# Performance work log

Measured on AMD Instinct MI355X. Metric: run time of the kernel, lower is better.

The kernel has to match this reference:

```python
import jax, jax.numpy as jnp
import numpy as np

N = 50000; E = 800000
IN = 128; H = 4; D = 32; OH = H * D; AIN = 2 * IN
SCALE = float(1.0 / np.sqrt(IN))

def _ln(x, g, b):
    m = jnp.mean(x, -1, keepdims=True)
    v = jnp.mean((x - m) ** 2, -1, keepdims=True)
    return (x - m) * jax.lax.rsqrt(v + 1e-5) * g + b

def setup_inputs():
    keys = iter(jax.random.split(jax.random.key(0), 24))
    nrm = lambda shape, s=1.0: jax.random.normal(next(keys), shape, dtype=jnp.float32) * s
    inp = {}
    inp['x0'] = nrm((N, IN)); inp['x1'] = nrm((N, IN)); inp['x99'] = nrm((N, AIN))
    inp['feat0'] = jax.random.uniform(next(keys), (E, 2), dtype=jnp.float32)
    inp['feat1'] = jax.random.uniform(next(keys), (E, 2), dtype=jnp.float32)
    for nm, shape in [('Wq', (IN, OH)), ('Wk', (IN, OH)), ('Wv', (IN, OH)), ('Wo', (OH, OH)), ('Wffn', (IN, OH)), ('Waq', (AIN, OH)), ('Wak', (AIN, OH)), ('Wav', (AIN, OH)), ('Wao', (OH, OH)), ('Waffn', (AIN, OH))]:
        inp[nm] = nrm(shape, 0.05)
    for nm in ['bq', 'bk', 'bv', 'bo', 'bffn', 'baq', 'bak', 'bav', 'bao', 'baffn', 'ln_b', 'aln_b']:
        inp[nm] = jnp.zeros((OH,), jnp.float32)
    inp['ln_g'] = jnp.ones((OH,), jnp.float32); inp['aln_g'] = jnp.ones((OH,), jnp.float32)
    for nm in ['src0', 'dst0', 'src1', 'dst1']:
        inp[nm] = jax.random.randint(next(keys), (E,), 0, N, dtype=jnp.int32)
    return inp

def _forward(x0, x1, x99, feat0, feat1, Wq, bq, Wk, bk, Wv, bv, Wo, bo, Wffn, bffn, ln_g, ln_b, Waq, baq, Wak, bak, Wav, bav, Wao, bao, Waffn, baffn, aln_g, aln_b, src0, dst0, src1, dst1):
    proj = lambda x, W, b: (x @ W + b).reshape(x.shape[0], H, D)
    xs = (x0, x1)
    edges = ((src0, dst0, feat0), (src1, dst1, feat1))
    q = [proj(x, Wq, bq) for x in xs]   # per-v_id linears are shared
    k = [proj(x, Wk, bk) for x in xs]
    v = [proj(x, Wv, bv) for x in xs]
    q99 = proj(x99, Waq, baq); k99 = proj(x99, Wak, bak); v99 = proj(x99, Wav, bav)
    aggr_outs = []
    for i, (src, dst, feat) in enumerate(edges):  # loop over the 2 edge types (structural)
        f = feat[:, None, 0:1]  # [E,1,1] 'connect' edge weight
        s = jnp.sum(k[i][src] * q[i][dst], -1, keepdims=True) * f   # [E,H,1]
        s99 = jnp.sum(k99[src] * q99[dst], -1, keepdims=True) * f
        s = jnp.exp(jnp.clip(s * SCALE, -5.0, 5.0))
        s99 = jnp.exp(jnp.clip(s99 * SCALE, -5.0, 5.0))
        wv = jax.ops.segment_sum(v[i][src] * s, dst, num_segments=N)    # [N,H,D]
        z = jax.ops.segment_sum(s, dst, num_segments=N)                 # [N,H,1]
        wv99 = jax.ops.segment_sum(v99[src] * s99, dst, num_segments=N)
        z99 = jax.ops.segment_sum(s99, dst, num_segments=N)
        # per-v_id branch (h_dict in original; computed but not returned by the module)
        o = (wv / (z + 1.0)).reshape(N, OH) @ Wo + bo
        h = xs[i] @ Wffn + bffn + o
        h = h + _ln(h, ln_g, ln_b)
        # aggregated (node 99) branch -> returned as aggr_h_dict[v_id]
        ao = (wv99 / (z99 + 1.0)).reshape(N, OH) @ Wao + bao
        ah = x99 @ Waffn + baffn + ao
        ah = ah + _ln(ah, aln_g, aln_b)
        aggr_outs.append(ah)
    return tuple(aggr_outs)

def reference(x0, x1, x99, feat0, feat1, Wq, bq, Wk, bk, Wv, bv, Wo, bo, Wffn, bffn, ln_g, ln_b, Waq, baq, Wak, bak, Wav, bav, Wao, bao, Waffn, baffn, aln_g, aln_b, src0, dst0, src1, dst1):
    return _forward(x0, x1, x99, feat0, feat1, Wq, bq, Wk, bk, Wv, bv, Wo, bo, Wffn, bffn, ln_g, ln_b, Waq, baq, Wak, bak, Wav, bav, Wao, bao, Waffn, baffn, aln_g, aln_b, src0, dst0, src1, dst1)
```

## Files before the change

### kernel.cpp

```cpp
#include <hip/hip_runtime.h>
#include <math.h>

#define NN 50000
#define EE 800000
#define AIN 256
#define OH 128

#define NTOT  (2 * NN)
#define NB    391
#define CAP   5120

typedef __attribute__((ext_vector_type(8))) short bf16x8;
typedef __attribute__((ext_vector_type(4))) float f32x4;

static __device__ __forceinline__ unsigned short f2bf(float f) {
    union { float f; unsigned int u; } v; v.f = f;
    return (unsigned short)((v.u + 0x7FFFu + ((v.u >> 16) & 1u)) >> 16);
}
static __device__ __forceinline__ float bflo(unsigned int u) { return __uint_as_float(u << 16); }
static __device__ __forceinline__ float bfhi(unsigned int u) { return __uint_as_float(u & 0xFFFF0000u); }

static __device__ __forceinline__ float foldpair(float a, float b, int mask, int lane) {
    const bool hi = (lane & mask) != 0;
    const float keep = hi ? b : a;
    const float send = hi ? a : b;
    return keep + __shfl_xor(send, mask);
}

__global__ __launch_bounds__(256) void cvt_x_k(const float* __restrict__ x, unsigned short* __restrict__ xb)
{
    const int i = blockIdx.x * 256 + threadIdx.x;
    if (i >= NN * AIN / 4) return;
    const float4 v = ((const float4*)x)[i];
    ushort4 o;
    o.x = f2bf(v.x); o.y = f2bf(v.y); o.z = f2bf(v.z); o.w = f2bf(v.w);
    ((ushort4*)xb)[i] = o;
}

__global__ __launch_bounds__(256) void cvt_w_k(
    const float* __restrict__ Wq, const float* __restrict__ Wk,
    const float* __restrict__ Wv, const float* __restrict__ Wf,
    const float* __restrict__ Wo, unsigned short* __restrict__ Wt,
    unsigned short* __restrict__ Waot)
{
    const int n = blockIdx.x;
    const int k = threadIdx.x;
    if (n < 512) {
        const float* W = (n < 128) ? Wq : (n < 256) ? Wk : (n < 384) ? Wv : Wf;
        Wt[(size_t)n * 256 + k] = f2bf(W[(size_t)k * OH + (n & 127)]);
    } else {
        if (k < 128) Waot[(size_t)(n - 512) * 128 + k] = f2bf(Wo[(size_t)k * OH + (n - 512)]);
    }
}

__global__ __launch_bounds__(256) void qkvf_mfma_k(
    const unsigned short* __restrict__ xb,
    const unsigned short* __restrict__ Wt,
    const float* __restrict__ bq, const float* __restrict__ bk,
    const float* __restrict__ bv, const float* __restrict__ bf,
    float* __restrict__ qf, unsigned short* __restrict__ kv,
    unsigned short* __restrict__ ffnb, int M)
{
    __shared__ unsigned short As[128][40];
    __shared__ unsigned short Bs[128][40];
    const int tid  = threadIdx.x;
    const int lane = tid & 63;
    const int wave = tid >> 6;
    const int wr = wave >> 1, wc = wave & 1;
    const int quad = lane >> 4, m16 = lane & 15;
    const int row0 = blockIdx.x * 128;
    const int col0 = blockIdx.y * 128;

    f32x4 acc[4][4];
    #pragma unroll
    for (int i = 0; i < 4; ++i)
        #pragma unroll
        for (int j = 0; j < 4; ++j) acc[i][j] = 0.f;

    const int lr  = tid >> 1;
    const int lkh = (tid & 1) * 16;

    for (int kt = 0; kt < 256; kt += 32) {
        uint4 a0 = {0,0,0,0}, a1 = {0,0,0,0};
        const int grow = row0 + lr;
        if (grow < M) {
            const uint4* p = (const uint4*)(xb + (size_t)grow * 256 + kt + lkh);
            a0 = p[0]; a1 = p[1];
        }
        *(uint4*)&As[lr][lkh]     = a0;
        *(uint4*)&As[lr][lkh + 8] = a1;
        const uint4* wp = (const uint4*)(Wt + (size_t)(col0 + lr) * 256 + kt + lkh);
        *(uint4*)&Bs[lr][lkh]     = wp[0];
        *(uint4*)&Bs[lr][lkh + 8] = wp[1];
        __syncthreads();
        bf16x8 af[4], bfr[4];
        #pragma unroll
        for (int t = 0; t < 4; ++t) af[t]  = *(const bf16x8*)&As[wr * 64 + t * 16 + m16][quad * 8];
        #pragma unroll
        for (int t = 0; t < 4; ++t) bfr[t] = *(const bf16x8*)&Bs[wc * 64 + t * 16 + m16][quad * 8];
        #pragma unroll
        for (int i = 0; i < 4; ++i)
            #pragma unroll
            for (int j = 0; j < 4; ++j)
                acc[i][j] = __builtin_amdgcn_mfma_f32_16x16x32_bf16(af[i], bfr[j], acc[i][j], 0, 0, 0);
        __syncthreads();
    }

    const int y = blockIdx.y;
    const float* bias = (y == 0) ? bq : (y == 1) ? bk : (y == 2) ? bv : bf;

    if (y == 0) {
        #pragma unroll
        for (int i = 0; i < 4; ++i)
            #pragma unroll
            for (int j = 0; j < 4; ++j) {
                const int col = wc * 64 + j * 16 + m16;
                const float b = bias[col];
                #pragma unroll
                for (int r = 0; r < 4; ++r) {
                    const int row = row0 + wr * 64 + i * 16 + quad * 4 + r;
                    if (row < M) qf[(size_t)row * 128 + col] = acc[i][j][r] + b;
                }
            }
    } else {
        unsigned short* obase = (y == 3) ? ffnb : kv;
        const int ostride = (y == 3) ? 128 : 256;
        const int ocol    = (y == 2) ? 128 : 0;
        #pragma unroll
        for (int i = 0; i < 4; ++i)
            #pragma unroll
            for (int j = 0; j < 4; ++j) {
                const int col = wc * 64 + j * 16 + m16;
                const float b = bias[col];
                #pragma unroll
                for (int r = 0; r < 4; ++r) {
                    const int row = row0 + wr * 64 + i * 16 + quad * 4 + r;
                    if (row < M) obase[(size_t)row * ostride + ocol + col] = f2bf(acc[i][j][r] + b);
                }
            }
    }
}

__global__ __launch_bounds__(256) void binpass_k(
    const int* __restrict__ dst0, const int* __restrict__ dst1,
    const int* __restrict__ src0, const int* __restrict__ src1,
    const float* __restrict__ feat0, const float* __restrict__ feat1,
    int* __restrict__ cursor, uint2* __restrict__ stage)
{
    __shared__ int hcnt[NB], blkbase[NB], lcur[NB];
    const int tid = threadIdx.x;
    const long base = (long)blockIdx.x * 8192;

    for (int i = tid; i < NB; i += 256) { hcnt[i] = 0; lcur[i] = 0; }
    __syncthreads();

    for (int i = tid; i < 8192; i += 256) {
        const long e = base + i;
        if (e < 2L * EE) {
            const int nid = (e < EE) ? dst0[e] : NN + dst1[e - EE];
            atomicAdd(&hcnt[nid >> 8], 1);
        }
    }
    __syncthreads();
    for (int i = tid; i < NB; i += 256)
        if (hcnt[i]) blkbase[i] = atomicAdd(&cursor[i], hcnt[i]);
    __syncthreads();

    for (int i = tid; i < 8192; i += 256) {
        const long e = base + i;
        if (e < 2L * EE) {
            const bool a = (e < EE);
            const int ee = a ? (int)e : (int)(e - EE);
            const int nid = a ? dst0[ee] : NN + dst1[ee];
            const int s = a ? src0[ee] : src1[ee];
            const float f = a ? feat0[(size_t)ee * 2] : feat1[(size_t)ee * 2];
            const int bk = nid >> 8;
            const int r = atomicAdd(&lcur[bk], 1);
            uint2 rec;
            rec.x = __float_as_uint(f);
            rec.y = ((unsigned int)s << 8) | (unsigned int)(nid & 255);
            stage[(size_t)bk * CAP + blkbase[bk] + r] = rec;
        }
    }
}

__global__ __launch_bounds__(512) void bscan_k(const int* __restrict__ cursor, int* __restrict__ bbase)
{
    __shared__ int part[512];
    const int t = threadIdx.x;
    const int v = (t < NB) ? cursor[t] : 0;
    part[t] = v;
    __syncthreads();
    for (int st = 1; st < 512; st <<= 1) {
        int u = (t >= st) ? part[t - st] : 0;
        __syncthreads();
        part[t] += u;
        __syncthreads();
    }
    if (t < NB) bbase[t] = part[t] - v;
}

__global__ __launch_bounds__(256) void sortpass_k(
    const uint2* __restrict__ stage, const int* __restrict__ cursor,
    const int* __restrict__ bbase, uint2* __restrict__ erec,
    int* __restrict__ off, int* __restrict__ deg)
{
    __shared__ int h[256], eb[256], cur[256];
    const int b = blockIdx.x;
    const int t = threadIdx.x;
    const int cntb = cursor[b];
    const int obase = bbase[b];
    const uint2* sb = stage + (size_t)b * CAP;

    h[t] = 0; cur[t] = 0;
    __syncthreads();
    for (int i = t; i < cntb; i += 256) atomicAdd(&h[(int)(sb[i].y & 255u)], 1);
    __syncthreads();
    eb[t] = h[t];
    __syncthreads();
    for (int st = 1; st < 256; st <<= 1) {
        int u = (t >= st) ? eb[t - st] : 0;
        __syncthreads();
        eb[t] += u;
        __syncthreads();
    }
    const int incl = eb[t];
    __syncthreads();
    eb[t] = incl - h[t];
    __syncthreads();

    const int nid = b * 256 + t;
    if (nid < NTOT) {
        off[nid] = obase + eb[t];
        deg[nid] = h[t];
    }

    for (int i = t; i < cntb; i += 256) {
        const uint2 r = sb[i];
        const int loc = (int)(r.y & 255u);
        const int rk = atomicAdd(&cur[loc], 1);
        uint2 o;
        o.x = r.y >> 8;
        o.y = r.x;
        erec[obase + eb[loc] + rk] = o;
    }
}

__global__ __launch_bounds__(256) void aggregate_k(
    const float* __restrict__ qf, const unsigned short* __restrict__ kv,
    const uint2* __restrict__ erec,
    const int* __restrict__ off, const int* __restrict__ deg,
    unsigned short* __restrict__ att)
{
    const int nid = blockIdx.x * 4 + (threadIdx.x >> 6);
    if (nid >= NTOT) return;
    const int n = (nid >= NN) ? nid - NN : nid;
    const int lane = threadIdx.x & 63;
    const int start = off[nid];
    const int count = deg[nid];

    const float2 q2 = *(const float2*)&qf[(size_t)n * 128 + 2 * lane];
    const float qx = q2.x, qy = q2.y;

    float accx = 0.f, accy = 0.f, zp = 0.f;
    const float SCALE = 0.088388347648318447f;
    const int slot = lane & 7;

    for (int base = 0; base < count; base += 64) {
        const int m = min(64, count - base);
        const uint2 rr = erec[start + base + min(lane, m - 1)];
        for (int j0 = 0; j0 < m; j0 += 8) {
            const int mb = min(8, m - j0);
            unsigned int ku[8], vu[8];
            #pragma unroll
            for (int s = 0; s < 8; ++s) {
                const int src = __shfl((int)rr.x, j0 + s);
                const unsigned short* kp = kv + (size_t)src * 256 + 2 * lane;
                ku[s] = *(const unsigned int*)kp;
                vu[s] = *(const unsigned int*)(kp + 128);
            }
            float p[8];
            #pragma unroll
            for (int s = 0; s < 8; ++s)
                p[s] = fmaf(bfhi(ku[s]), qy, bflo(ku[s]) * qx);
            float r01 = foldpair(p[0], p[1], 1, lane);
            float r23 = foldpair(p[2], p[3], 1, lane);
            float r45 = foldpair(p[4], p[5], 1, lane);
            float r67 = foldpair(p[6], p[7], 1, lane);
            float r03 = foldpair(r01, r23, 2, lane);
            float r47 = foldpair(r45, r67, 2, lane);
            float r07 = foldpair(r03, r47, 4, lane);
            r07 += __shfl_xor(r07, 8);
            const float f = __int_as_float(__shfl((int)rr.y, j0 + slot));
            float sc = __expf(fminf(5.f, fmaxf(-5.f, r07 * f * SCALE)));
            if (slot >= mb) sc = 0.f;
            zp += sc;
            #pragma unroll
            for (int s = 0; s < 8; ++s) {
                const float scb = __shfl(sc, (lane & 48) + s);
                accx = fmaf(bflo(vu[s]), scb, accx);
                accy = fmaf(bfhi(vu[s]), scb, accy);
            }
        }
    }
    float z = zp;
    z += __shfl_xor(z, 1);
    z += __shfl_xor(z, 2);
    z += __shfl_xor(z, 4);

    const float inv = 1.f / (z + 1.f);
    const unsigned int o = ((unsigned int)f2bf(accy * inv) << 16) | (unsigned int)f2bf(accx * inv);
    *(unsigned int*)(att + (size_t)nid * 128 + 2 * lane) = o;
}

__global__ __launch_bounds__(256) void attn_out_mfma_k(
    const unsigned short* __restrict__ attAll, const unsigned short* __restrict__ Wt,
    const float* __restrict__ bo, const unsigned short* __restrict__ ffnb,
    const float* __restrict__ g, const float* __restrict__ bln,
    float* __restrict__ Yall, int M)
{
    __shared__ unsigned short As[128][40];
    __shared__ unsigned short Bs[128][40];
    __shared__ float rsum[2][128], rsq[2][128];
    __shared__ float meanar[128], invar[128];

    const unsigned short* att = attAll + (size_t)blockIdx.y * NN * 128;
    float* Y = Yall + (size_t)blockIdx.y * NN * 128;

    const int tid  = threadIdx.x;
    const int lane = tid & 63;
    const int wave = tid >> 6;
    const int wr = wave >> 1, wc = wave & 1;
    const int quad = lane >> 4, m16 = lane & 15;
    const int row0 = blockIdx.x * 128;

    f32x4 acc[4][4];
    #pragma unroll
    for (int i = 0; i < 4; ++i)
        #pragma unroll
        for (int j = 0; j < 4; ++j) acc[i][j] = 0.f;

    const int lr  = tid >> 1;
    const int lkh = (tid & 1) * 16;

    for (int kt = 0; kt < 128; kt += 32) {
        uint4 a0 = {0,0,0,0}, a1 = {0,0,0,0};
        const int grow = row0 + lr;
        if (grow < M) {
            const uint4* p = (const uint4*)(att + (size_t)grow * 128 + kt + lkh);
            a0 = p[0]; a1 = p[1];
        }
        *(uint4*)&As[lr][lkh]     = a0;
        *(uint4*)&As[lr][lkh + 8] = a1;
        const uint4* wp = (const uint4*)(Wt + (size_t)lr * 128 + kt + lkh);
        *(uint4*)&Bs[lr][lkh]     = wp[0];
        *(uint4*)&Bs[lr][lkh + 8] = wp[1];
        __syncthreads();
        bf16x8 af[4], bfr[4];
        #pragma unroll
        for (int t = 0; t < 4; ++t) af[t]  = *(const bf16x8*)&As[wr * 64 + t * 16 + m16][quad * 8];
        #pragma unroll
        for (int t = 0; t < 4; ++t) bfr[t] = *(const bf16x8*)&Bs[wc * 64 + t * 16 + m16][quad * 8];
        #pragma unroll
        for (int i = 0; i < 4; ++i)
            #pragma unroll
            for (int j = 0; j < 4; ++j)
                acc[i][j] = __builtin_amdgcn_mfma_f32_16x16x32_bf16(af[i], bfr[j], acc[i][j], 0, 0, 0);
        __syncthreads();
    }

    #pragma unroll
    for (int i = 0; i < 4; ++i) {
        #pragma unroll
        for (int r = 0; r < 4; ++r) {
            const int rl = wr * 64 + i * 16 + quad * 4 + r;
            const int grow = row0 + rl;
            float s = 0.f, q = 0.f;
            #pragma unroll
            for (int j = 0; j < 4; ++j) {
                const int col = wc * 64 + j * 16 + m16;
                float v = acc[i][j][r] + bo[col];
                if (grow < M) v += bflo(ffnb[(size_t)grow * 128 + col]);
                acc[i][j][r] = v;
                s += v; q += v * v;
            }
            #pragma unroll
            for (int mm = 1; mm <= 8; mm <<= 1) {
                s += __shfl_xor(s, mm, 16);
                q += __shfl_xor(q, mm, 16);
            }
            if (m16 == 0) { rsum[wc][rl] = s; rsq[wc][rl] = q; }
        }
    }
    __syncthreads();
    if (tid < 128) {
        const float s = rsum[0][tid] + rsum[1][tid];
        const float q = rsq[0][tid] + rsq[1][tid];
        const float mean = s * (1.f / 128.f);
        const float var  = q * (1.f / 128.f) - mean * mean;
        meanar[tid] = mean;
        invar[tid]  = rsqrtf(fmaxf(var, 0.f) + 1e-5f);
    }
    __syncthreads();

    #pragma unroll
    for (int i = 0; i < 4; ++i) {
        #pragma unroll
        for (int j = 0; j < 4; ++j) {
            const int col = wc * 64 + j * 16 + m16;
            const float gv = g[col], lv = bln[col];
            #pragma unroll
            for (int r = 0; r < 4; ++r) {
                const int rl = wr * 64 + i * 16 + quad * 4 + r;
                const int grow = row0 + rl;
                if (grow < M) {
                    const float v = acc[i][j][r];
                    Y[(size_t)grow * 128 + col] = v + (v - meanar[rl]) * invar[rl] * gv + lv;
                }
            }
        }
    }
}

extern "C" void kernel_launch(void* const* d_in, const int* in_sizes, int n_in,
                              void* d_out, int out_size, void* d_ws, size_t ws_size,
                              hipStream_t stream) {
    const float* x99   = (const float*)d_in[2];
    const float* feat0 = (const float*)d_in[3];
    const float* feat1 = (const float*)d_in[4];
    const float* Waq   = (const float*)d_in[10];
    const float* Wak   = (const float*)d_in[11];
    const float* Wav   = (const float*)d_in[12];
    const float* Wao   = (const float*)d_in[13];
    const float* Waffn = (const float*)d_in[14];
    const float* baq   = (const float*)d_in[20];
    const float* bak   = (const float*)d_in[21];
    const float* bav   = (const float*)d_in[22];
    const float* bao   = (const float*)d_in[23];
    const float* baffn = (const float*)d_in[24];
    const float* aln_b = (const float*)d_in[26];
    const float* aln_g = (const float*)d_in[28];
    const int* src0 = (const int*)d_in[29];
    const int* dst0 = (const int*)d_in[30];
    const int* src1 = (const int*)d_in[31];
    const int* dst1 = (const int*)d_in[32];

    unsigned short* xb   = (unsigned short*)d_ws;
    float*          qf   = (float*)(xb + (size_t)NN * 256);
    unsigned short* kv   = (unsigned short*)(qf + (size_t)NN * 128);
    unsigned short* ffnb = kv   + (size_t)NN * 256;
    unsigned short* att  = ffnb + (size_t)NN * 128;
    unsigned short* Wt   = att  + (size_t)NTOT * 128;
    unsigned short* Waot = Wt   + (size_t)512 * 256;
    int* cursor = (int*)(Waot + 128 * 128);
    int* bbase  = cursor + NB;
    int* off    = bbase + NB;
    int* deg    = off + NTOT;

    float* out = (float*)d_out;
    uint2* stage = (uint2*)d_out;
    uint2* erec  = stage + (size_t)NB * CAP;

    cvt_x_k<<<(NN * AIN / 4 + 255) / 256, 256, 0, stream>>>(x99, xb);
    cvt_w_k<<<640, 256, 0, stream>>>(Waq, Wak, Wav, Waffn, Wao, Wt, Waot);

    const int mtiles = (NN + 127) / 128;
    qkvf_mfma_k<<<dim3(mtiles, 4), 256, 0, stream>>>(xb, Wt, baq, bak, bav, baffn, qf, kv, ffnb, NN);

    hipMemsetAsync(cursor, 0, NB * sizeof(int), stream);
    binpass_k<<<(2 * EE + 8191) / 8192, 256, 0, stream>>>(
        dst0, dst1, src0, src1, feat0, feat1, cursor, stage);
    bscan_k<<<1, 512, 0, stream>>>(cursor, bbase);
    sortpass_k<<<NB, 256, 0, stream>>>(stage, cursor, bbase, erec, off, deg);

    aggregate_k<<<(NTOT + 3) / 4, 256, 0, stream>>>(qf, kv, erec, off, deg, att);
    attn_out_mfma_k<<<dim3(mtiles, 2), 256, 0, stream>>>(att, Waot, bao, ffnb, aln_g, aln_b, out, NN);
}
```

Before: 474.4 us.

## Process four edges per wavefront with 16-lane groups and prefetch next K/V rows

```diff
diff --git a/kernel.cpp b/kernel.cpp
--- a/kernel.cpp
+++ b/kernel.cpp
@@ -19,13 +19,6 @@
 }
 static __device__ __forceinline__ float bflo(unsigned int u) { return __uint_as_float(u << 16); }
 static __device__ __forceinline__ float bfhi(unsigned int u) { return __uint_as_float(u & 0xFFFF0000u); }
-
-static __device__ __forceinline__ float foldpair(float a, float b, int mask, int lane) {
-    const bool hi = (lane & mask) != 0;
-    const float keep = hi ? b : a;
-    const float send = hi ? a : b;
-    return keep + __shfl_xor(send, mask);
-}
 
 __global__ __launch_bounds__(256) void cvt_x_k(const float* __restrict__ x, unsigned short* __restrict__ xb)
 {
@@ -256,61 +249,83 @@
     if (nid >= NTOT) return;
     const int n = (nid >= NN) ? nid - NN : nid;
     const int lane = threadIdx.x & 63;
+    const int g   = lane >> 4;
+    const int d16 = lane & 15;
     const int start = off[nid];
     const int count = deg[nid];
 
-    const float2 q2 = *(const float2*)&qf[(size_t)n * 128 + 2 * lane];
-    const float qx = q2.x, qy = q2.y;
-
-    float accx = 0.f, accy = 0.f, zp = 0.f;
+    const float4* qp = (const float4*)(qf + (size_t)n * 128 + d16 * 8);
+    const float4 qa = qp[0];
+    const float4 qb = qp[1];
+
+    float a0 = 0.f, a1 = 0.f, a2 = 0.f, a3 = 0.f;
+    float a4 = 0.f, a5 = 0.f, a6 = 0.f, a7 = 0.f;
+    float zp = 0.f;
     const float SCALE = 0.088388347648318447f;
-    const int slot = lane & 7;
+    const unsigned short* kvl = kv + d16 * 8;
 
     for (int base = 0; base < count; base += 64) {
         const int m = min(64, count - base);
         const uint2 rr = erec[start + base + min(lane, m - 1)];
-        for (int j0 = 0; j0 < m; j0 += 8) {
-            const int mb = min(8, m - j0);
-            unsigned int ku[8], vu[8];
-            #pragma unroll
-            for (int s = 0; s < 8; ++s) {
-                const int src = __shfl((int)rr.x, j0 + s);
-                const unsigned short* kp = kv + (size_t)src * 256 + 2 * lane;
-                ku[s] = *(const unsigned int*)kp;
-                vu[s] = *(const unsigned int*)(kp + 128);
-            }
-            float p[8];
-            #pragma unroll
-            for (int s = 0; s < 8; ++s)
-                p[s] = fmaf(bfhi(ku[s]), qy, bflo(ku[s]) * qx);
-            float r01 = foldpair(p[0], p[1], 1, lane);
-            float r23 = foldpair(p[2], p[3], 1, lane);
-            float r45 = foldpair(p[4], p[5], 1, lane);
-            float r67 = foldpair(p[6], p[7], 1, lane);
-            float r03 = foldpair(r01, r23, 2, lane);
-            float r47 = foldpair(r45, r67, 2, lane);
-            float r07 = foldpair(r03, r47, 4, lane);
-            r07 += __shfl_xor(r07, 8);
-            const float f = __int_as_float(__shfl((int)rr.y, j0 + slot));
-            float sc = __expf(fminf(5.f, fmaxf(-5.f, r07 * f * SCALE)));
-            if (slot >= mb) sc = 0.f;
+        int src = __shfl((int)rr.x, g);
+        const uint4* p0 = (const uint4*)(kvl + (size_t)src * 256);
+        uint4 kc = p0[0];
+        uint4 vc = p0[16];
+        for (int j0 = 0; j0 < m; j0 += 4) {
+            const uint4 kk = kc, vv = vc;
+            const float f = __int_as_float(__shfl((int)rr.y, j0 + g));
+            const int jn = j0 + 4;
+            if (jn < m) {
+                src = __shfl((int)rr.x, jn + g);
+                const uint4* pn = (const uint4*)(kvl + (size_t)src * 256);
+                kc = pn[0];
+                vc = pn[16];
+            }
+            float p =        bflo(kk.x) * qa.x;
+            p = fmaf(bfhi(kk.x), qa.y, p);
+            p = fmaf(bflo(kk.y), qa.z, p);
+            p = fmaf(bfhi(kk.y), qa.w, p);
+            p = fmaf(bflo(kk.z), qb.x, p);
+            p = fmaf(bfhi(kk.z), qb.y, p);
+            p = fmaf(bflo(kk.w), qb.z, p);
+            p = fmaf(bfhi(kk.w), qb.w, p);
+            p += __shfl_xor(p, 1);
+            p += __shfl_xor(p, 2);
+            float sc = __expf(fminf(5.f, fmaxf(-5.f, p * f * SCALE)));
+            sc = (j0 + g < m) ? sc : 0.f;
             zp += sc;
-            #pragma unroll
-            for (int s = 0; s < 8; ++s) {
-                const float scb = __shfl(sc, (lane & 48) + s);
-                accx = fmaf(bflo(vu[s]), scb, accx);
-                accy = fmaf(bfhi(vu[s]), scb, accy);
-            }
-        }
-    }
+            a0 = fmaf(bflo(vv.x), sc, a0);
+            a1 = fmaf(bfhi(vv.x), sc, a1);
+            a2 = fmaf(bflo(vv.y), sc, a2);
+            a3 = fmaf(bfhi(vv.y), sc, a3);
+            a4 = fmaf(bflo(vv.z), sc, a4);
+            a5 = fmaf(bfhi(vv.z), sc, a5);
+            a6 = fmaf(bflo(vv.w), sc, a6);
+            a7 = fmaf(bfhi(vv.w), sc, a7);
+        }
+    }
+
     float z = zp;
-    z += __shfl_xor(z, 1);
-    z += __shfl_xor(z, 2);
-    z += __shfl_xor(z, 4);
+    z += __shfl_xor(z, 16);
+    z += __shfl_xor(z, 32);
+    a0 += __shfl_xor(a0, 16); a0 += __shfl_xor(a0, 32);
+    a1 += __shfl_xor(a1, 16); a1 += __shfl_xor(a1, 32);
+    a2 += __shfl_xor(a2, 16); a2 += __shfl_xor(a2, 32);
+    a3 += __shfl_xor(a3, 16); a3 += __shfl_xor(a3, 32);
+    a4 += __shfl_xor(a4, 16); a4 += __shfl_xor(a4, 32);
+    a5 += __shfl_xor(a5, 16); a5 += __shfl_xor(a5, 32);
+    a6 += __shfl_xor(a6, 16); a6 += __shfl_xor(a6, 32);
+    a7 += __shfl_xor(a7, 16); a7 += __shfl_xor(a7, 32);
 
     const float inv = 1.f / (z + 1.f);
-    const unsigned int o = ((unsigned int)f2bf(accy * inv) << 16) | (unsigned int)f2bf(accx * inv);
-    *(unsigned int*)(att + (size_t)nid * 128 + 2 * lane) = o;
+    const float e0 = (g & 1) ? a2 : a0;
+    const float e1 = (g & 1) ? a3 : a1;
+    const float e2 = (g & 1) ? a6 : a4;
+    const float e3 = (g & 1) ? a7 : a5;
+    const float ax = ((g & 2) ? e2 : e0) * inv;
+    const float ay = ((g & 2) ? e3 : e1) * inv;
+    const unsigned int o = ((unsigned int)f2bf(ay) << 16) | (unsigned int)f2bf(ax);
+    *(unsigned int*)(att + (size_t)nid * 128 + d16 * 8 + g * 2) = o;
 }
 
 __global__ __launch_bounds__(256) void attn_out_mfma_k(
```

After: 476.4 us. Within noise of the previous version (+0.4%).
